# Performance work log

Measured on AMD Instinct MI355X. Metric: run time of the kernel, lower is better.

The kernel has to match this reference:

```python
import jax, jax.numpy as jnp
import numpy as np

B, T, D = 2, 2048, 2048
N, K, H = 16, 8, 128  # heads, kv heads, head_dim
F = 8192              # ffn hidden


def _apply_rope(x, positions, max_wavelength=10000):
    # x: [B, L, heads, H]; positions: [B, L]
    half = x.shape[-1] // 2
    freq_exponents = (2.0 / x.shape[-1]) * jnp.arange(half, dtype=jnp.float32)
    timescale = max_wavelength ** freq_exponents
    radians = positions.astype(jnp.float32)[..., None] / timescale[None, None, :]
    radians = radians[..., None, :]  # [B, L, 1, half]
    sin, cos = jnp.sin(radians), jnp.cos(radians)
    x1, x2 = jnp.split(x, 2, axis=-1)
    return jnp.concatenate([x1 * cos - x2 * sin, x2 * cos + x1 * sin], axis=-1)


def _rms_norm(x, scale):
    var = jnp.mean(jnp.square(x), axis=-1, keepdims=True)
    return x * jax.lax.rsqrt(var + 1e-6) * (1 + scale)


def setup_inputs() -> dict:
    key = jax.random.key(0)
    ks = jax.random.split(key, 8)
    s = 0.02
    x = jax.random.normal(ks[0], (B, T, D), jnp.float32)
    positions = jnp.broadcast_to(jnp.arange(T, dtype=jnp.int32)[None, :], (B, T))
    causal = jnp.tril(jnp.ones((T, T), dtype=bool))
    attn_mask = jnp.broadcast_to(causal[None, None, :, :], (B, 1, T, T))
    return {
        "x": x,
        "positions": positions,
        "attn_mask": attn_mask,
        "w_q": jax.random.normal(ks[1], (N, D, H), jnp.float32) * s,
        "w_kv": jax.random.normal(ks[2], (2, K, D, H), jnp.float32) * s,
        "w_attn_vec": jax.random.normal(ks[3], (N, H, D), jnp.float32) * s,
        "scale_pre_attn": jax.random.normal(ks[4], (D,), jnp.float32) * s,
        "scale_pre_ffw": jax.random.normal(ks[5], (D,), jnp.float32) * s,
        "w_gating": jax.random.normal(ks[6], (2, D, F), jnp.float32) * s,
        "w_linear": jax.random.normal(ks[7], (F, D), jnp.float32) * s,
    }


def reference(x, positions, attn_mask, w_q, w_kv, w_attn_vec,
              scale_pre_attn, scale_pre_ffw, w_gating, w_linear):
    # pre-attention RMSNorm
    xn = _rms_norm(x, scale_pre_attn)

    # GQA projections
    q = jnp.einsum('BTD,NDH->BTNH', xn, w_q)
    kv = jnp.einsum('BSD,eKDH->eBSKH', xn, w_kv)
    k, v = kv[0], kv[1]

    q = _apply_rope(q, positions) * (H ** -0.5)
    k = _apply_rope(k, positions)

    G = N // K
    q = q.reshape(q.shape[0], q.shape[1], K, G, H)  # B T K G H
    logits = jnp.einsum('BTKGH,BSKH->BKGTS', q, k).astype(jnp.float32)
    big_neg = -2.3819763e38
    masked = jnp.where(attn_mask[:, :, None, :, :], logits, big_neg)
    probs = jax.nn.softmax(masked, axis=-1).astype(k.dtype)
    enc = jnp.einsum('BKGTS,BSKH->BTKGH', probs, v)
    enc = enc.reshape(enc.shape[0], enc.shape[1], N, H)
    attn_out = jnp.einsum('BTNH,NHD->BTD', enc, w_attn_vec)

    # residual + pre-FFN RMSNorm + GeGLU FFN
    residual = x + attn_out
    h = _rms_norm(residual, scale_pre_ffw)
    gate = jax.nn.gelu(jnp.dot(h, w_gating[0]))
    act = gate * jnp.dot(h, w_gating[1])
    out = residual + jnp.dot(act, w_linear)
    return out
```

## Files before the change

### kernel.cpp

```cpp
#include <hip/hip_runtime.h>
#include <hip/hip_bf16.h>


typedef __attribute__((ext_vector_type(8))) short bf16x8;
typedef __attribute__((ext_vector_type(4))) float f32x4;

#define GLP(p) ((const __attribute__((address_space(1))) void*)(p))
#define LDSP(p) ((__attribute__((address_space(3))) void*)(p))

__device__ __forceinline__ float bf2f(unsigned short h) {
  union { unsigned int u; float f; } v; v.u = ((unsigned int)h) << 16; return v.f;
}
__device__ __forceinline__ unsigned short f2bf(float f) {
  union { float f; unsigned int u; } v; v.f = f;
  unsigned int r = v.u + 0x7fffu + ((v.u >> 16) & 1u);
  return (unsigned short)(r >> 16);
}
__device__ __forceinline__ float gelu_f(float x) {
  float t = tanhf(0.7978845608028654f * (x + 0.044715f * x * x * x));
  return 0.5f * x * (1.f + t);
}

template <int IN_F32>
__global__ __launch_bounds__(256) void rmsnorm_kernel(const void* __restrict__ x_,
                                                      const float* __restrict__ scale,
                                                      unsigned short* __restrict__ out) {
  int row = blockIdx.x, tid = threadIdx.x;
  float f[8]; float ss = 0.f;
  if (IN_F32) {
    const float* xr = (const float*)x_ + (size_t)row * 2048 + tid * 8;
#pragma unroll
    for (int i = 0; i < 8; ++i) { f[i] = xr[i]; ss += f[i] * f[i]; }
  } else {
    const unsigned short* xr = (const unsigned short*)x_ + (size_t)row * 2048;
    bf16x8 xv = *(const bf16x8*)(xr + tid * 8);
#pragma unroll
    for (int i = 0; i < 8; ++i) { f[i] = bf2f((unsigned short)xv[i]); ss += f[i] * f[i]; }
  }
#pragma unroll
  for (int off = 32; off >= 1; off >>= 1) ss += __shfl_xor(ss, off);
  __shared__ float red[4];
  if ((tid & 63) == 0) red[tid >> 6] = ss;
  __syncthreads();
  ss = red[0] + red[1] + red[2] + red[3];
  float r = rsqrtf(ss * (1.f / 2048.f) + 1e-6f);
  const float* sv = scale + tid * 8;
  bf16x8 o;
#pragma unroll
  for (int i = 0; i < 8; ++i) o[i] = (short)f2bf(f[i] * r * (1.f + sv[i]));
  *(bf16x8*)(out + (size_t)row * 2048 + tid * 8) = o;
}

__global__ __launch_bounds__(256) void transpose_cast_kernel(const float* __restrict__ in,
                                                             unsigned short* __restrict__ out,
                                                             int R, int C, long ibs, long obs) {
  __shared__ float tile[32][33];
  int z = blockIdx.z;
  const float* ip = in + (size_t)z * ibs;
  unsigned short* op = out + (size_t)z * obs;
  int c0 = blockIdx.x * 32, r0 = blockIdx.y * 32;
  int tx = threadIdx.x, ty = threadIdx.y;
#pragma unroll
  for (int i = 0; i < 32; i += 8)
    tile[ty + i][tx] = ip[(size_t)(r0 + ty + i) * C + (c0 + tx)];
  __syncthreads();
#pragma unroll
  for (int i = 0; i < 32; i += 8)
    op[(size_t)(c0 + ty + i) * R + (r0 + tx)] = f2bf(tile[tx][ty + i]);
}

__global__ __launch_bounds__(256) void vtrans_kernel(const unsigned short* __restrict__ qkv,
                                                     unsigned short* __restrict__ vT) {
  __shared__ unsigned short tile[32][33];
  int z = blockIdx.z, bb = z >> 3, kh = z & 7;
  int s0 = blockIdx.x * 32, h0 = blockIdx.y * 32;
  int tx = threadIdx.x, ty = threadIdx.y;
  const unsigned short* ip = qkv + ((size_t)bb * 2048) * 4096 + 3072 + kh * 128;
  unsigned short* op = vT + (size_t)z * 128 * 2048;
#pragma unroll
  for (int i = 0; i < 32; i += 8)
    tile[ty + i][tx] = ip[(size_t)(s0 + ty + i) * 4096 + h0 + tx];
  __syncthreads();
#pragma unroll
  for (int i = 0; i < 32; i += 8)
    op[(size_t)(h0 + ty + i) * 2048 + s0 + tx] = tile[tx][ty + i];
}

template <int MODE, int OUT_F32, int ADD_F32>
__global__ __launch_bounds__(256, 2) void gemm_bt(const unsigned short* __restrict__ A, int lda,
                                                  const unsigned short* __restrict__ BT, int Kd,
                                                  int Ncols, void* __restrict__ out_,
                                                  const void* __restrict__ add_) {
  __shared__ unsigned short sA[128 * 32];
  __shared__ unsigned short sB[128 * 32];
  int tid = threadIdx.x;
  int lane = tid & 63, wave = tid >> 6;
  int quad = lane >> 4, l16 = lane & 15;
  int wr = (wave >> 1) * 64, wc = (wave & 1) * 64;
  long rowBase = (long)blockIdx.y * 128, colBase = (long)blockIdx.x * 128;
  f32x4 acc[4][4];
#pragma unroll
  for (int i = 0; i < 4; ++i)
#pragma unroll
    for (int j = 0; j < 4; ++j) acc[i][j] = (f32x4){0.f, 0.f, 0.f, 0.f};

  const unsigned short* Ag = A + (rowBase + (tid >> 2)) * (size_t)lda + (tid & 3) * 8;
  const unsigned short* Bg = BT + (colBase + (tid >> 2)) * (size_t)Kd + (tid & 3) * 8;
  unsigned short* sAw = sA + wave * 512;
  unsigned short* sBw = sB + wave * 512;

  for (int kt = 0; kt < Kd; kt += 32) {
    __syncthreads();
    __builtin_amdgcn_global_load_lds(GLP(Ag), LDSP(sAw), 16, 0, 0);
    __builtin_amdgcn_global_load_lds(GLP(Ag + (size_t)64 * lda), LDSP(sAw + 2048), 16, 0, 0);
    __builtin_amdgcn_global_load_lds(GLP(Bg), LDSP(sBw), 16, 0, 0);
    __builtin_amdgcn_global_load_lds(GLP(Bg + (size_t)64 * Kd), LDSP(sBw + 2048), 16, 0, 0);
    Ag += 32; Bg += 32;
    __syncthreads();
    bf16x8 af[4], bfr[4];
#pragma unroll
    for (int i = 0; i < 4; ++i) af[i] = *(const bf16x8*)(sA + (wr + i * 16 + l16) * 32 + quad * 8);
#pragma unroll
    for (int j = 0; j < 4; ++j) bfr[j] = *(const bf16x8*)(sB + (wc + j * 16 + l16) * 32 + quad * 8);
#pragma unroll
    for (int i = 0; i < 4; ++i)
#pragma unroll
      for (int j = 0; j < 4; ++j)
        acc[i][j] = __builtin_amdgcn_mfma_f32_16x16x32_bf16(af[i], bfr[j], acc[i][j], 0, 0, 0);
  }
  float* outf = (float*)out_;
  unsigned short* outb = (unsigned short*)out_;
  const float* addf = (const float*)add_;
  const unsigned short* addb = (const unsigned short*)add_;
#pragma unroll
  for (int i = 0; i < 4; ++i)
#pragma unroll
    for (int j = 0; j < 4; ++j)
#pragma unroll
      for (int r = 0; r < 4; ++r) {
        long row = rowBase + wr + i * 16 + quad * 4 + r;
        long col = colBase + wc + j * 16 + l16;
        long idx = row * (long)Ncols + col;
        float v = acc[i][j][r];
        if (MODE == 1) v += (ADD_F32 ? addf[idx] : bf2f(addb[idx]));
        if (MODE == 2) v = gelu_f(bf2f(addb[idx])) * v;
        if (OUT_F32) outf[idx] = v; else outb[idx] = f2bf(v);
      }
}

__global__ __launch_bounds__(256) void rope_kernel(unsigned short* __restrict__ qkv,
                                                   const int* __restrict__ pos) {
  int gid = blockIdx.x * 256 + threadIdx.x;
  int hp = gid & 63;
  int rh = gid >> 6;
  int row = rh / 24;
  int head = rh - row * 24;
  float p = (float)pos[row];
  long cb; float sc;
  if (head < 16) { cb = (long)head * 128; sc = 0.08838834764831845f; }
  else { cb = 2048 + (long)(head - 16) * 128; sc = 1.f; }
  unsigned short* ptr = qkv + (long)row * 4096 + cb;
  float inv = exp2f(-(float)hp * (13.287712379549449f / 64.f));
  float ang = p * inv;
  float s = sinf(ang), c = cosf(ang);
  float x1 = bf2f(ptr[hp]), x2 = bf2f(ptr[hp + 64]);
  ptr[hp]      = f2bf((x1 * c - x2 * s) * sc);
  ptr[hp + 64] = f2bf((x2 * c + x1 * s) * sc);
}

__global__ __launch_bounds__(256, 2) void attn_kernel(const unsigned short* __restrict__ qkv,
                                                      const unsigned short* __restrict__ vT,
                                                      unsigned short* __restrict__ enc) {
  extern __shared__ char smem[];
  unsigned short* sK = (unsigned short*)smem;
  unsigned short* sVT = sK + 64 * 128;
  float* sS = (float*)(smem + 32768);
  unsigned short* sP = (unsigned short*)(smem + 32768 + 16896);
  float* sM = (float*)(smem + 32768 + 16896 + 9216);
  float* sL = sM + 64;
  float* sAl = sL + 64;

  int qt = blockIdx.x, n = blockIdx.y, b = blockIdx.z;
  int tid = threadIdx.x, lane = tid & 63, w = tid >> 6;
  int quad = lane >> 4, l16 = lane & 15;
  int kh = n >> 1;
  long rowQ = (long)b * 2048 + (long)qt * 64;

  bf16x8 qf[4];
  {
    const unsigned short* qp = qkv + (rowQ + w * 16 + l16) * 4096 + n * 128 + quad * 8;
#pragma unroll
    for (int ks = 0; ks < 4; ++ks) qf[ks] = *(const bf16x8*)(qp + ks * 32);
  }
  if (tid < 64) { sM[tid] = -1e30f; sL[tid] = 0.f; }
  f32x4 oacc[8];
#pragma unroll
  for (int t = 0; t < 8; ++t) oacc[t] = (f32x4){0.f, 0.f, 0.f, 0.f};

  int srow = tid >> 2, cg = tid & 3;

  for (int st = 0; st <= qt; ++st) {
    __syncthreads();
#pragma unroll
    for (int it = 0; it < 4; ++it) {
      int idx = it * 256 + tid;
      int r = idx >> 4, c = idx & 15;
      bf16x8 kv8 = *(const bf16x8*)(qkv + ((long)b * 2048 + st * 64 + r) * 4096 + 2048 + kh * 128 + c * 8);
      *(bf16x8*)(sK + r * 128 + ((c ^ (r & 7)) * 8)) = kv8;
    }
#pragma unroll
    for (int it = 0; it < 4; ++it) {
      int idx = it * 256 + tid;
      int h = idx >> 3, c = idx & 7;
      bf16x8 vv8 = *(const bf16x8*)(vT + ((long)(b * 8 + kh) * 128 + h) * 2048 + st * 64 + c * 8);
      *(bf16x8*)(sVT + h * 64 + ((c ^ (h & 7)) * 8)) = vv8;
    }
    __syncthreads();

    f32x4 sacc[4];
#pragma unroll
    for (int nt = 0; nt < 4; ++nt) sacc[nt] = (f32x4){0.f, 0.f, 0.f, 0.f};
#pragma unroll
    for (int ks = 0; ks < 4; ++ks)
#pragma unroll
      for (int nt = 0; nt < 4; ++nt) {
        int r = nt * 16 + l16;
        bf16x8 kf = *(const bf16x8*)(sK + r * 128 + (((ks * 4 + quad) ^ (r & 7)) * 8));
        sacc[nt] = __builtin_amdgcn_mfma_f32_16x16x32_bf16(qf[ks], kf, sacc[nt], 0, 0, 0);
      }
#pragma unroll
    for (int nt = 0; nt < 4; ++nt)
#pragma unroll
      for (int r = 0; r < 4; ++r)
        sS[(w * 16 + quad * 4 + r) * 66 + nt * 16 + l16] = sacc[nt][r];
    __syncthreads();

    float vals[16];
    int tglob = qt * 64 + srow;
    float mx = -1e30f;
#pragma unroll
    for (int j = 0; j < 16; ++j) {
      int col = cg * 16 + j;
      float v = sS[srow * 66 + col];
      if (st * 64 + col > tglob) v = -1e30f;
      vals[j] = v;
      mx = fmaxf(mx, v);
    }
    mx = fmaxf(mx, __shfl_xor(mx, 1));
    mx = fmaxf(mx, __shfl_xor(mx, 2));
    float m_old = sM[srow], l_old = sL[srow];
    float m_new = fmaxf(m_old, mx);
    float alpha = __expf(m_old - m_new);
    float sum = 0.f;
#pragma unroll
    for (int j = 0; j < 16; ++j) { vals[j] = __expf(vals[j] - m_new); sum += vals[j]; }
    sum += __shfl_xor(sum, 1);
    sum += __shfl_xor(sum, 2);
    float l_new = alpha * l_old + sum;
    __syncthreads();

#pragma unroll
    for (int jj = 0; jj < 8; ++jj) {
      unsigned int pk = (unsigned int)f2bf(vals[2 * jj]) | ((unsigned int)f2bf(vals[2 * jj + 1]) << 16);
      *(unsigned int*)(sP + srow * 72 + cg * 16 + jj * 2) = pk;
    }
    if (cg == 0) { sM[srow] = m_new; sL[srow] = l_new; sAl[srow] = alpha; }
    __syncthreads();

#pragma unroll
    for (int r = 0; r < 4; ++r) {
      float al = sAl[w * 16 + quad * 4 + r];
#pragma unroll
      for (int nt = 0; nt < 8; ++nt) oacc[nt][r] *= al;
    }
#pragma unroll
    for (int ks = 0; ks < 2; ++ks) {
      bf16x8 pf = *(const bf16x8*)(sP + (w * 16 + l16) * 72 + ks * 32 + quad * 8);
#pragma unroll
      for (int nt = 0; nt < 8; ++nt) {
        int hh = nt * 16 + l16;
        bf16x8 vf = *(const bf16x8*)(sVT + hh * 64 + (((ks * 4 + quad) ^ (hh & 7)) * 8));
        oacc[nt] = __builtin_amdgcn_mfma_f32_16x16x32_bf16(pf, vf, oacc[nt], 0, 0, 0);
      }
    }
  }

#pragma unroll
  for (int r = 0; r < 4; ++r) {
    float invl = 1.f / sL[w * 16 + quad * 4 + r];
    long trow = rowQ + w * 16 + quad * 4 + r;
#pragma unroll
    for (int nt = 0; nt < 8; ++nt)
      enc[trow * 2048 + n * 128 + nt * 16 + l16] = f2bf(oacc[nt][r] * invl);
  }
}

extern "C" void kernel_launch(void* const* d_in, const int* in_sizes, int n_in,
                              void* d_out, int out_size, void* d_ws, size_t ws_size,
                              hipStream_t stream) {
  const float* x = (const float*)d_in[0];
  const int* positions = (const int*)d_in[1];
  const float* wq = (const float*)d_in[3];
  const float* wkv = (const float*)d_in[4];
  const float* wav = (const float*)d_in[5];
  const float* s_attn = (const float*)d_in[6];
  const float* s_ffw = (const float*)d_in[7];
  const float* wg = (const float*)d_in[8];
  const float* wl = (const float*)d_in[9];
  float* outp = (float*)d_out;

  char* ws = (char*)d_ws;
  size_t o = 0;
  unsigned short* XN = (unsigned short*)(ws + o);    o += (size_t)4096 * 2048 * 2;
  unsigned short* WQKVT = (unsigned short*)(ws + o); o += (size_t)4096 * 2048 * 2;
  unsigned short* WAVT = (unsigned short*)(ws + o);  o += (size_t)2048 * 2048 * 2;
  unsigned short* WGT = (unsigned short*)(ws + o);   o += (size_t)8192 * 2048 * 2;
  unsigned short* QKV = (unsigned short*)(ws + o);   o += (size_t)4096 * 4096 * 2;
  unsigned short* VTb = (unsigned short*)(ws + o);   o += (size_t)16 * 128 * 2048 * 2;
  unsigned short* GATE = (unsigned short*)(ws + o);  o += (size_t)4096 * 8192 * 2;
  unsigned short* ENC = WQKVT;
  unsigned short* RES = QKV;
  unsigned short* HB = XN;

  dim3 b256(256), bT(32, 8);

  rmsnorm_kernel<1><<<4096, b256, 0, stream>>>(x, s_attn, XN);

  transpose_cast_kernel<<<dim3(4, 64, 16), bT, 0, stream>>>(wq, WQKVT, 2048, 128, 262144L, 262144L);
  transpose_cast_kernel<<<dim3(4, 64, 8), bT, 0, stream>>>(wkv, WQKVT + (size_t)2048 * 2048, 2048, 128, 262144L, 262144L);
  transpose_cast_kernel<<<dim3(4, 64, 8), bT, 0, stream>>>(wkv + (size_t)8 * 262144, WQKVT + (size_t)3072 * 2048, 2048, 128, 262144L, 262144L);
  transpose_cast_kernel<<<dim3(64, 64, 1), bT, 0, stream>>>(wav, WAVT, 2048, 2048, 0L, 0L);

  gemm_bt<0, 0, 0><<<dim3(32, 32), b256, 0, stream>>>(XN, 2048, WQKVT, 2048, 4096, QKV, nullptr);

  vtrans_kernel<<<dim3(64, 4, 16), bT, 0, stream>>>(QKV, VTb);

  rope_kernel<<<24576, b256, 0, stream>>>(QKV, positions);

  attn_kernel<<<dim3(32, 16, 2), b256, 59648, stream>>>(QKV, VTb, ENC);

  gemm_bt<1, 0, 1><<<dim3(16, 32), b256, 0, stream>>>(ENC, 2048, WAVT, 2048, 2048, RES, x);

  rmsnorm_kernel<0><<<4096, b256, 0, stream>>>(RES, s_ffw, HB);

  transpose_cast_kernel<<<dim3(256, 64, 1), bT, 0, stream>>>(wg, WGT, 2048, 8192, 0L, 0L);
  gemm_bt<0, 0, 0><<<dim3(64, 32), b256, 0, stream>>>(HB, 2048, WGT, 2048, 8192, GATE, nullptr);

  transpose_cast_kernel<<<dim3(256, 64, 1), bT, 0, stream>>>(wg + (size_t)2048 * 8192, WGT, 2048, 8192, 0L, 0L);
  gemm_bt<2, 0, 0><<<dim3(64, 32), b256, 0, stream>>>(HB, 2048, WGT, 2048, 8192, GATE, GATE);

  transpose_cast_kernel<<<dim3(64, 256, 1), bT, 0, stream>>>(wl, WGT, 8192, 2048, 0L, 0L);
  gemm_bt<1, 1, 0><<<dim3(16, 32), b256, 0, stream>>>(GATE, 8192, WGT, 8192, 2048, outp, RES);
}
```

Measured before the change: 1.179 ms.

## Fuse gate and up GEMMs into one dual-accumulator GeGLU kernel

Replaces the two separate gating GEMMs (the first writing GATE, the second rereading it to apply gelu and multiply) with one kernel that computes both projections against a shared A tile and writes gelu(g)*u directly. The FFN is split into two halves of 4096 columns so both transposed weight slices fit in the existing workspace. This removes one full write and read of the 4096x8192 bf16 intermediate and halves the A-operand loads. In exchange it doubles the accumulator registers per thread (launch_bounds set to 2 blocks per SM), which can reduce occupancy or cause spills.

```diff
diff --git a/kernel.cpp b/kernel.cpp
--- a/kernel.cpp
+++ b/kernel.cpp
@@ -53,7 +53,7 @@
 
 __global__ __launch_bounds__(256) void transpose_cast_kernel(const float* __restrict__ in,
                                                              unsigned short* __restrict__ out,
-                                                             int R, int C, long ibs, long obs) {
+                                                             int R, int ldi, long ibs, long obs) {
   __shared__ float tile[32][33];
   int z = blockIdx.z;
   const float* ip = in + (size_t)z * ibs;
@@ -62,7 +62,7 @@
   int tx = threadIdx.x, ty = threadIdx.y;
 #pragma unroll
   for (int i = 0; i < 32; i += 8)
-    tile[ty + i][tx] = ip[(size_t)(r0 + ty + i) * C + (c0 + tx)];
+    tile[ty + i][tx] = ip[(size_t)(r0 + ty + i) * ldi + (c0 + tx)];
   __syncthreads();
 #pragma unroll
   for (int i = 0; i < 32; i += 8)
@@ -143,8 +143,73 @@
         long idx = row * (long)Ncols + col;
         float v = acc[i][j][r];
         if (MODE == 1) v += (ADD_F32 ? addf[idx] : bf2f(addb[idx]));
-        if (MODE == 2) v = gelu_f(bf2f(addb[idx])) * v;
         if (OUT_F32) outf[idx] = v; else outb[idx] = f2bf(v);
+      }
+}
+
+__global__ __launch_bounds__(256, 2) void gemm_gating(const unsigned short* __restrict__ A,
+                                                      const unsigned short* __restrict__ BgT,
+                                                      const unsigned short* __restrict__ BuT,
+                                                      unsigned short* __restrict__ act,
+                                                      long colOfs) {
+  __shared__ unsigned short sA[128 * 32];
+  __shared__ unsigned short sBg[128 * 32];
+  __shared__ unsigned short sBu[128 * 32];
+  int tid = threadIdx.x;
+  int lane = tid & 63, wave = tid >> 6;
+  int quad = lane >> 4, l16 = lane & 15;
+  int wr = (wave >> 1) * 64, wc = (wave & 1) * 64;
+  long rowBase = (long)blockIdx.y * 128, colBase = (long)blockIdx.x * 128;
+  f32x4 gacc[4][4], uacc[4][4];
+#pragma unroll
+  for (int i = 0; i < 4; ++i)
+#pragma unroll
+    for (int j = 0; j < 4; ++j) {
+      gacc[i][j] = (f32x4){0.f, 0.f, 0.f, 0.f};
+      uacc[i][j] = (f32x4){0.f, 0.f, 0.f, 0.f};
+    }
+
+  const unsigned short* Ag  = A + (rowBase + (tid >> 2)) * (size_t)2048 + (tid & 3) * 8;
+  const unsigned short* Bgg = BgT + (colBase + (tid >> 2)) * (size_t)2048 + (tid & 3) * 8;
+  const unsigned short* Bug = BuT + (colBase + (tid >> 2)) * (size_t)2048 + (tid & 3) * 8;
+  unsigned short* sAw = sA + wave * 512;
+  unsigned short* sBgw = sBg + wave * 512;
+  unsigned short* sBuw = sBu + wave * 512;
+
+  for (int kt = 0; kt < 2048; kt += 32) {
+    __syncthreads();
+    __builtin_amdgcn_global_load_lds(GLP(Ag), LDSP(sAw), 16, 0, 0);
+    __builtin_amdgcn_global_load_lds(GLP(Ag + (size_t)64 * 2048), LDSP(sAw + 2048), 16, 0, 0);
+    __builtin_amdgcn_global_load_lds(GLP(Bgg), LDSP(sBgw), 16, 0, 0);
+    __builtin_amdgcn_global_load_lds(GLP(Bgg + (size_t)64 * 2048), LDSP(sBgw + 2048), 16, 0, 0);
+    __builtin_amdgcn_global_load_lds(GLP(Bug), LDSP(sBuw), 16, 0, 0);
+    __builtin_amdgcn_global_load_lds(GLP(Bug + (size_t)64 * 2048), LDSP(sBuw + 2048), 16, 0, 0);
+    Ag += 32; Bgg += 32; Bug += 32;
+    __syncthreads();
+    bf16x8 af[4], bg[4], bu[4];
+#pragma unroll
+    for (int i = 0; i < 4; ++i) af[i] = *(const bf16x8*)(sA + (wr + i * 16 + l16) * 32 + quad * 8);
+#pragma unroll
+    for (int j = 0; j < 4; ++j) bg[j] = *(const bf16x8*)(sBg + (wc + j * 16 + l16) * 32 + quad * 8);
+#pragma unroll
+    for (int j = 0; j < 4; ++j) bu[j] = *(const bf16x8*)(sBu + (wc + j * 16 + l16) * 32 + quad * 8);
+#pragma unroll
+    for (int i = 0; i < 4; ++i)
+#pragma unroll
+      for (int j = 0; j < 4; ++j) {
+        gacc[i][j] = __builtin_amdgcn_mfma_f32_16x16x32_bf16(af[i], bg[j], gacc[i][j], 0, 0, 0);
+        uacc[i][j] = __builtin_amdgcn_mfma_f32_16x16x32_bf16(af[i], bu[j], uacc[i][j], 0, 0, 0);
+      }
+  }
+#pragma unroll
+  for (int i = 0; i < 4; ++i)
+#pragma unroll
+    for (int j = 0; j < 4; ++j)
+#pragma unroll
+      for (int r = 0; r < 4; ++r) {
+        long row = rowBase + wr + i * 16 + quad * 4 + r;
+        long col = colBase + wc + j * 16 + l16;
+        act[row * 8192 + colOfs + col] = f2bf(gelu_f(gacc[i][j][r]) * uacc[i][j][r]);
       }
 }
 
@@ -317,7 +382,7 @@
   unsigned short* WGT = (unsigned short*)(ws + o);   o += (size_t)8192 * 2048 * 2;
   unsigned short* QKV = (unsigned short*)(ws + o);   o += (size_t)4096 * 4096 * 2;
   unsigned short* VTb = (unsigned short*)(ws + o);   o += (size_t)16 * 128 * 2048 * 2;
-  unsigned short* GATE = (unsigned short*)(ws + o);  o += (size_t)4096 * 8192 * 2;
+  unsigned short* ACT = (unsigned short*)(ws + o);   o += (size_t)4096 * 8192 * 2;
   unsigned short* ENC = WQKVT;
   unsigned short* RES = QKV;
   unsigned short* HB = XN;
@@ -343,12 +408,14 @@
 
   rmsnorm_kernel<0><<<4096, b256, 0, stream>>>(RES, s_ffw, HB);
 
-  transpose_cast_kernel<<<dim3(256, 64, 1), bT, 0, stream>>>(wg, WGT, 2048, 8192, 0L, 0L);
-  gemm_bt<0, 0, 0><<<dim3(64, 32), b256, 0, stream>>>(HB, 2048, WGT, 2048, 8192, GATE, nullptr);
-
-  transpose_cast_kernel<<<dim3(256, 64, 1), bT, 0, stream>>>(wg + (size_t)2048 * 8192, WGT, 2048, 8192, 0L, 0L);
-  gemm_bt<2, 0, 0><<<dim3(64, 32), b256, 0, stream>>>(HB, 2048, WGT, 2048, 8192, GATE, GATE);
+  for (int half = 0; half < 2; ++half) {
+    long f0 = (long)half * 4096;
+    transpose_cast_kernel<<<dim3(128, 64, 1), bT, 0, stream>>>(wg + f0, WGT, 2048, 8192, 0L, 0L);
+    transpose_cast_kernel<<<dim3(128, 64, 1), bT, 0, stream>>>(wg + (size_t)2048 * 8192 + f0,
+                                                               WGT + (size_t)4096 * 2048, 2048, 8192, 0L, 0L);
+    gemm_gating<<<dim3(32, 32), b256, 0, stream>>>(HB, WGT, WGT + (size_t)4096 * 2048, ACT, f0);
+  }
 
   transpose_cast_kernel<<<dim3(64, 256, 1), bT, 0, stream>>>(wl, WGT, 8192, 2048, 0L, 0L);
-  gemm_bt<1, 1, 0><<<dim3(16, 32), b256, 0, stream>>>(GATE, 8192, WGT, 8192, 2048, outp, RES);
-}
+  gemm_bt<1, 1, 0><<<dim3(16, 32), b256, 0, stream>>>(ACT, 8192, WGT, 8192, 2048, outp, RES);
+}
```

After: 1.155 ms. 1.02x faster.
